# Kernel optimization log

Hardware: AMD Instinct MI355X
Metric: run time of the kernel (lower is better)

Reference implementation:

```python
import jax, jax.numpy as jnp
import numpy as np

N = 100000   # nodes
E = 1600000  # edges (avg degree 16)
D = 64       # feature / hidden / embedding dim
OUT = 2
NEG_SLOPE = 0.2


def setup_inputs() -> dict:
    key = jax.random.key(0)
    ks = jax.random.split(key, 12)
    s = 1.0 / np.sqrt(D)
    return {
        "x": jax.random.normal(ks[0], (N, D), dtype=jnp.float32),
        "edge_index": jax.random.randint(ks[1], (2, E), 0, N, dtype=jnp.int64),
        "Wl": jax.random.normal(ks[2], (3, D, D), dtype=jnp.float32) * s,
        "bl": jnp.zeros((3, D), dtype=jnp.float32),
        "Wr": jax.random.normal(ks[3], (3, D, D), dtype=jnp.float32) * s,
        "br": jnp.zeros((3, D), dtype=jnp.float32),
        "att": jax.random.normal(ks[4], (3, D), dtype=jnp.float32) * s,
        "bg": jnp.zeros((3, D), dtype=jnp.float32),
        "Ws": jax.random.normal(ks[5], (3, D, D), dtype=jnp.float32) * s,
        "bs": jnp.zeros((3, D), dtype=jnp.float32),
        "Wout": jax.random.normal(ks[6], (D, OUT), dtype=jnp.float32) * s,
        "bout": jnp.zeros((OUT,), dtype=jnp.float32),
    }


def _gatv2(h, src, dst, Wl, bl, Wr, br, att, bg):
    # GATv2Conv (heads=1, concat, add_self_loops=False):
    #   e_ij = att . LeakyReLU(Wl h_j + Wr h_i); softmax over incoming edges of i;
    #   out_i = sum_j alpha_ij * (Wl h_j) + bias
    xl = h @ Wl + bl                      # [N, D] source transform
    xr = h @ Wr + br                      # [N, D] dest transform
    e = jax.nn.leaky_relu(xl[src] + xr[dst], NEG_SLOPE) @ att  # [E]
    m = jax.ops.segment_max(e, dst, num_segments=N)            # per-dest max
    a = jnp.exp(e - m[dst])                                    # [E]
    denom = jax.ops.segment_sum(a, dst, num_segments=N)        # [N]
    alpha = a / denom[dst]                                     # [E]
    agg = jax.ops.segment_sum(alpha[:, None] * xl[src], dst, num_segments=N)
    return agg + bg                                            # [N, D]


def reference(x, edge_index, Wl, bl, Wr, br, att, bg, Ws, bs, Wout, bout):
    src, dst = edge_index[0], edge_index[1]
    # layer 1: gat1 + skip1, relu (dropout_rate=0 -> identity)
    h = jax.nn.relu(_gatv2(x, src, dst, Wl[0], bl[0], Wr[0], br[0], att[0], bg[0])
                    + x @ Ws[0] + bs[0])
    # middle layer
    h = jax.nn.relu(_gatv2(h, src, dst, Wl[1], bl[1], Wr[1], br[1], att[1], bg[1])
                    + h @ Ws[1] + bs[1])
    # last gat layer: no relu after
    h = _gatv2(h, src, dst, Wl[2], bl[2], Wr[2], br[2], att[2], bg[2]) + h @ Ws[2] + bs[2]
    return h @ Wout + bout
```

## Files before the change

kernel.cpp:

```cpp
#include <hip/hip_runtime.h>
#include <stdint.h>

#define NN 100000
#define EE 1600000
#define DD 64
#define NBUCK 391
#define SCWG 200
#define SCCHUNK 8000

using short8 = __attribute__((ext_vector_type(8))) short;
using f32x4  = __attribute__((ext_vector_type(4))) float;
using f2     = __attribute__((ext_vector_type(2))) float;


__device__ __forceinline__ unsigned short bf16_rne(float f) {
    unsigned int u = __float_as_uint(f);
    unsigned int r = (u + 0x7FFFu + ((u >> 16) & 1u)) >> 16;
    return (unsigned short)r;
}
__device__ __forceinline__ float bf16_to_f32(unsigned short h) {
    return __uint_as_float(((unsigned int)h) << 16);
}


__global__ void bucket_hist(const int* __restrict__ dst, int* __restrict__ bhist) {
    __shared__ int h[NBUCK];
    int t = threadIdx.x;
    for (int b = t; b < NBUCK; b += 256) h[b] = 0;
    __syncthreads();
    int start = blockIdx.x * SCCHUNK;
    int endi = min(start + SCCHUNK, EE);
    for (int e = start + t; e < endi; e += 256)
        atomicAdd(&h[dst[e] >> 8], 1);
    __syncthreads();
    for (int b = t; b < NBUCK; b += 256)
        if (h[b]) atomicAdd(&bhist[b], h[b]);
}

__global__ void bucket_scan(const int* __restrict__ bhist, int* __restrict__ bbase,
                            int* __restrict__ bcursor, int* __restrict__ offsets) {
    __shared__ int s[512];
    int t = threadIdx.x;
    int v = (t < NBUCK) ? bhist[t] : 0;
    s[t] = v;
    __syncthreads();
    for (int off = 1; off < 512; off <<= 1) {
        int a = (t >= off) ? s[t - off] : 0;
        __syncthreads();
        s[t] += a;
        __syncthreads();
    }
    if (t < NBUCK) { int excl = s[t] - v; bbase[t] = excl; bcursor[t] = excl; }
    if (t == 0) { bbase[NBUCK] = EE; offsets[NN] = EE; }
}

__global__ void bucket_scatter(const int* __restrict__ src, const int* __restrict__ dst,
                               int* __restrict__ bcursor, unsigned int* __restrict__ bedges) {
    __shared__ int cnt[NBUCK];
    __shared__ int lcur[NBUCK];
    int t = threadIdx.x;
    for (int b = t; b < NBUCK; b += 256) cnt[b] = 0;
    __syncthreads();
    int start = blockIdx.x * SCCHUNK;
    int endi = min(start + SCCHUNK, EE);
    for (int e = start + t; e < endi; e += 256)
        atomicAdd(&cnt[dst[e] >> 8], 1);
    __syncthreads();
    for (int b = t; b < NBUCK; b += 256) {
        int c = cnt[b];
        lcur[b] = c ? atomicAdd(&bcursor[b], c) : 0;
    }
    __syncthreads();
    for (int e = start + t; e < endi; e += 256) {
        int d = dst[e];
        int pos = atomicAdd(&lcur[d >> 8], 1);
        bedges[pos] = ((unsigned int)(d & 255) << 24) | (unsigned int)src[e];
    }
}

__global__ void bucket_csr(const unsigned int* __restrict__ bedges, const int* __restrict__ bbase,
                           int* __restrict__ offsets, int* __restrict__ csr) {
    __shared__ int ncnt[256];
    __shared__ int lofs[256];
    int b = blockIdx.x;
    int t = threadIdx.x;
    int beg = bbase[b], endb = bbase[b + 1];
    ncnt[t] = 0;
    __syncthreads();
    for (int e = beg + t; e < endb; e += 256)
        atomicAdd(&ncnt[bedges[e] >> 24], 1);
    __syncthreads();
    int v = ncnt[t];
    lofs[t] = v;
    __syncthreads();
    for (int off = 1; off < 256; off <<= 1) {
        int a = (t >= off) ? lofs[t - off] : 0;
        __syncthreads();
        lofs[t] += a;
        __syncthreads();
    }
    int excl = lofs[t] - v;
    int node = b * 256 + t;
    if (node < NN) offsets[node] = beg + excl;
    __syncthreads();
    ncnt[t] = beg + excl;
    __syncthreads();
    for (int e = beg + t; e < endb; e += 256) {
        unsigned int ed = bedges[e];
        int pos = atomicAdd(&ncnt[ed >> 24], 1);
        csr[pos] = (int)(ed & 0xFFFFFFu);
    }
}


__global__ void conv_wx(const float* __restrict__ Wl, const float* __restrict__ Wr,
                        const float* __restrict__ Ws, const float* __restrict__ x,
                        unsigned short* __restrict__ Wt_hi, unsigned short* __restrict__ Wt_lo,
                        unsigned short* __restrict__ Ahi) {
    if (blockIdx.x < 144) {
        int e = blockIdx.x * 256 + threadIdx.x;
        if (e >= 9 * 4096) return;
        int mat = e >> 12;
        int r   = e & 4095;
        int k   = r >> 6, n = r & 63;
        int L = mat / 3, j = mat % 3;
        const float* W = (j == 0) ? Wl : ((j == 1) ? Wr : Ws);
        float v = W[L * 4096 + k * 64 + n];
        unsigned short hi = bf16_rne(v);
        unsigned short lo = bf16_rne(v - bf16_to_f32(hi));
        Wt_hi[mat * 4096 + n * 64 + k] = hi;
        Wt_lo[mat * 4096 + n * 64 + k] = lo;
    } else {
        int i = (blockIdx.x - 144) * 256 + threadIdx.x;
        int total = NN * 16;
        int stride = (gridDim.x - 144) * 256;
        for (; i < total; i += stride) {
            float4 v = *(const float4*)&x[(size_t)i * 4];
            ushort4 h;
            h.x = bf16_rne(v.x);
            h.y = bf16_rne(v.y);
            h.z = bf16_rne(v.z);
            h.w = bf16_rne(v.w);
            *(ushort4*)&Ahi[(size_t)i * 4] = h;
        }
    }
}


__global__ __launch_bounds__(256) void gemm_mfma(
    const unsigned short* __restrict__ Ahi,
    const unsigned short* __restrict__ Wt_hi, const unsigned short* __restrict__ Wt_lo,
    const float* __restrict__ bl, const float* __restrict__ br, const float* __restrict__ bs,
    unsigned short* __restrict__ Xlb, unsigned short* __restrict__ XRS) {
    int lane = threadIdx.x & 63;
    int wid  = threadIdx.x >> 6;
    int m0 = (blockIdx.x * 4 + wid) * 32;
    if (m0 >= NN) return;

    int l4 = lane & 15;
    int hi = lane >> 4;
    int koff = hi * 8;

    int arow0 = m0 + l4, arow1 = m0 + 16 + l4;
    bool ok0 = arow0 < NN, ok1 = arow1 < NN;
    int ar0 = ok0 ? arow0 : NN - 1;
    int ar1 = ok1 ? arow1 : NN - 1;

    const unsigned short* ab0 = Ahi + (size_t)ar0 * 64;
    const unsigned short* ab1 = Ahi + (size_t)ar1 * 64;
    short8 a0k0 = *(const short8*)(ab0 + koff);
    short8 a0k1 = *(const short8*)(ab0 + 32 + koff);
    short8 a1k0 = *(const short8*)(ab1 + koff);
    short8 a1k1 = *(const short8*)(ab1 + 32 + koff);

    int nbase0 = hi * 4;

#pragma unroll
    for (int m = 0; m < 3; m++) {
        const unsigned short* wh = Wt_hi + m * 4096;
        const unsigned short* wl = Wt_lo + m * 4096;
        const float* bias = (m == 0) ? bl : ((m == 1) ? br : bs);
#pragma unroll
        for (int tt = 0; tt < 4; tt++) {
            int ncol = tt * 16 + l4;
            const unsigned short* bh = wh + ncol * 64 + koff;
            const unsigned short* blo = wl + ncol * 64 + koff;
            short8 bhi0 = *(const short8*)bh;
            short8 bhi1 = *(const short8*)(bh + 32);
            short8 blo0 = *(const short8*)blo;
            short8 blo1 = *(const short8*)(blo + 32);

            f32x4 acc0 = {0.f, 0.f, 0.f, 0.f};
            f32x4 acc1 = {0.f, 0.f, 0.f, 0.f};
            acc0 = __builtin_amdgcn_mfma_f32_16x16x32_bf16(bhi0, a0k0, acc0, 0, 0, 0);
            acc1 = __builtin_amdgcn_mfma_f32_16x16x32_bf16(bhi0, a1k0, acc1, 0, 0, 0);
            acc0 = __builtin_amdgcn_mfma_f32_16x16x32_bf16(bhi1, a0k1, acc0, 0, 0, 0);
            acc1 = __builtin_amdgcn_mfma_f32_16x16x32_bf16(bhi1, a1k1, acc1, 0, 0, 0);
            acc0 = __builtin_amdgcn_mfma_f32_16x16x32_bf16(blo0, a0k0, acc0, 0, 0, 0);
            acc1 = __builtin_amdgcn_mfma_f32_16x16x32_bf16(blo0, a1k0, acc1, 0, 0, 0);
            acc0 = __builtin_amdgcn_mfma_f32_16x16x32_bf16(blo1, a0k1, acc0, 0, 0, 0);
            acc1 = __builtin_amdgcn_mfma_f32_16x16x32_bf16(blo1, a1k1, acc1, 0, 0, 0);

            int nb = tt * 16 + nbase0;
            float4 bb = *(const float4*)&bias[nb];
            ushort4 h0, h1;
            h0.x = bf16_rne(acc0[0] + bb.x); h0.y = bf16_rne(acc0[1] + bb.y);
            h0.z = bf16_rne(acc0[2] + bb.z); h0.w = bf16_rne(acc0[3] + bb.w);
            h1.x = bf16_rne(acc1[0] + bb.x); h1.y = bf16_rne(acc1[1] + bb.y);
            h1.z = bf16_rne(acc1[2] + bb.z); h1.w = bf16_rne(acc1[3] + bb.w);
            if (m == 0) {
                if (ok0) *(ushort4*)&Xlb[(size_t)ar0 * 64 + nb] = h0;
                if (ok1) *(ushort4*)&Xlb[(size_t)ar1 * 64 + nb] = h1;
            } else {
                int coff = (m == 1) ? 0 : 64;
                if (ok0) *(ushort4*)&XRS[(size_t)ar0 * 128 + coff + nb] = h0;
                if (ok1) *(ushort4*)&XRS[(size_t)ar1 * 128 + coff + nb] = h1;
            }
        }
    }
}


__device__ __forceinline__ float group_sum16(float t) {
    t += __int_as_float(__builtin_amdgcn_update_dpp(0, __float_as_int(t), 0xB1, 0xF, 0xF, true));
    t += __int_as_float(__builtin_amdgcn_update_dpp(0, __float_as_int(t), 0x4E, 0xF, 0xF, true));
    t += __int_as_float(__builtin_amdgcn_update_dpp(0, __float_as_int(t), 0x141, 0xF, 0xF, true));
    t += __int_as_float(__builtin_amdgcn_update_dpp(0, __float_as_int(t), 0x140, 0xF, 0xF, true));
    return t;
}

__device__ __forceinline__ void unpack4(uint2 u, f2& v01, f2& v23) {
    v01 = f2{ __uint_as_float(u.x << 16), __uint_as_float(u.x & 0xFFFF0000u) };
    v23 = f2{ __uint_as_float(u.y << 16), __uint_as_float(u.y & 0xFFFF0000u) };
}

__global__ __launch_bounds__(256) void node_kernel(
    const unsigned short* __restrict__ Xlb, const unsigned short* __restrict__ XRS,
    const int* __restrict__ offsets, const int* __restrict__ csr,
    const float* __restrict__ att, const float* __restrict__ bg,
    unsigned short* __restrict__ hout, int do_relu,
    const float* __restrict__ Wout, const float* __restrict__ bout,
    float* __restrict__ outp, int do_out) {
    int lane = threadIdx.x & 63;
    int wid  = threadIdx.x >> 6;
    int i = blockIdx.x * 4 + wid;
    if (i >= NN) return;
    int sub = lane & 15;
    int grp = lane >> 4;

    f2 xr01, xr23;
    unpack4(*(const uint2*)&XRS[(size_t)i * 128 + sub * 4], xr01, xr23);
    float4 att4 = *(const float4*)&att[sub * 4];
    f2 at01 = {att4.x, att4.y}, at23 = {att4.z, att4.w};

    f2 agg01 = {0.f, 0.f}, agg23 = {0.f, 0.f};
    float denom = 0.f;
    int beg = offsets[i], end = offsets[i + 1];

    for (int j0 = beg; j0 < end; j0 += 8) {
        int jA = j0 + grp, jB = jA + 4;
        bool vA = jA < end, vB = jB < end;
        int sA = csr[vA ? jA : beg];
        int sB = csr[vB ? jB : beg];
        uint2 uA = *(const uint2*)&Xlb[(size_t)sA * 64 + sub * 4];
        uint2 uB = *(const uint2*)&Xlb[(size_t)sB * 64 + sub * 4];
        f2 xA01, xA23, xB01, xB23;
        unpack4(uA, xA01, xA23);
        unpack4(uB, xB01, xB23);

        f2 sA01 = xA01 + xr01;
        f2 sA23 = xA23 + xr23;
        f2 sB01 = xB01 + xr01;
        f2 sB23 = xB23 + xr23;
        f2 lA01 = { fmaxf(sA01.x, 0.2f * sA01.x), fmaxf(sA01.y, 0.2f * sA01.y) };
        f2 lA23 = { fmaxf(sA23.x, 0.2f * sA23.x), fmaxf(sA23.y, 0.2f * sA23.y) };
        f2 lB01 = { fmaxf(sB01.x, 0.2f * sB01.x), fmaxf(sB01.y, 0.2f * sB01.y) };
        f2 lB23 = { fmaxf(sB23.x, 0.2f * sB23.x), fmaxf(sB23.y, 0.2f * sB23.y) };

        f2 tAv = lA01 * at01 + lA23 * at23;
        f2 tBv = lB01 * at01 + lB23 * at23;
        float tA = group_sum16(tAv.x + tAv.y);
        float tB = group_sum16(tBv.x + tBv.y);
        float aA = vA ? __expf(tA) : 0.f;
        float aB = vB ? __expf(tB) : 0.f;

        f2 aAv = {aA, aA};
        f2 aBv = {aB, aB};
        agg01 += aAv * xA01 + aBv * xB01;
        agg23 += aAv * xA23 + aBv * xB23;
        denom += aA + aB;
    }

    float aggx = agg01.x, aggy = agg01.y, aggz = agg23.x, aggw = agg23.y;
#pragma unroll
    for (int m = 16; m <= 32; m <<= 1) {
        aggx  += __shfl_xor(aggx, m, 64);
        aggy  += __shfl_xor(aggy, m, 64);
        aggz  += __shfl_xor(aggz, m, 64);
        aggw  += __shfl_xor(aggw, m, 64);
        denom += __shfl_xor(denom, m, 64);
    }

    float inv = (denom > 0.f) ? (1.0f / denom) : 0.f;
    f2 sk01, sk23;
    unpack4(*(const uint2*)&XRS[(size_t)i * 128 + 64 + sub * 4], sk01, sk23);
    float4 bg4 = *(const float4*)&bg[sub * 4];
    float4 res;
    res.x = aggx * inv + bg4.x + sk01.x;
    res.y = aggy * inv + bg4.y + sk01.y;
    res.z = aggz * inv + bg4.z + sk23.x;
    res.w = aggw * inv + bg4.w + sk23.y;
    if (do_relu) {
        res.x = fmaxf(res.x, 0.f); res.y = fmaxf(res.y, 0.f);
        res.z = fmaxf(res.z, 0.f); res.w = fmaxf(res.w, 0.f);
    }
    if (do_out) {
        float4 w01 = *(const float4*)&Wout[8 * sub];
        float4 w23 = *(const float4*)&Wout[8 * sub + 4];
        float o0 = res.x * w01.x + res.y * w01.z + res.z * w23.x + res.w * w23.z;
        float o1 = res.x * w01.y + res.y * w01.w + res.z * w23.y + res.w * w23.w;
        o0 = group_sum16(o0);
        o1 = group_sum16(o1);
        if (lane == 0) {
            outp[(size_t)i * 2 + 0] = o0 + bout[0];
            outp[(size_t)i * 2 + 1] = o1 + bout[1];
        }
    } else {
        if (grp == 0) {
            ushort4 h;
            h.x = bf16_rne(res.x);
            h.y = bf16_rne(res.y);
            h.z = bf16_rne(res.z);
            h.w = bf16_rne(res.w);
            *(ushort4*)&hout[(size_t)i * 64 + sub * 4] = h;
        }
    }
}


extern "C" void kernel_launch(void* const* d_in, const int* in_sizes, int n_in,
                              void* d_out, int out_size, void* d_ws, size_t ws_size,
                              hipStream_t stream) {
    const float* x    = (const float*)d_in[0];
    const int*   ei   = (const int*)d_in[1];
    const float* Wl   = (const float*)d_in[2];
    const float* bl   = (const float*)d_in[3];
    const float* Wr   = (const float*)d_in[4];
    const float* br   = (const float*)d_in[5];
    const float* att  = (const float*)d_in[6];
    const float* bg   = (const float*)d_in[7];
    const float* Ws   = (const float*)d_in[8];
    const float* bs   = (const float*)d_in[9];
    const float* Wout = (const float*)d_in[10];
    const float* bout = (const float*)d_in[11];
    float* out = (float*)d_out;

    size_t off = 0;
    char* base = (char*)d_ws;
    auto alloc = [&](size_t bytes) -> void* {
        void* p = base + off;
        off += (bytes + 255) & ~(size_t)255;
        return p;
    };
    unsigned short* Xlb = (unsigned short*)alloc((size_t)NN * 64 * 2);
    unsigned short* XRS = (unsigned short*)alloc((size_t)NN * 128 * 2);
    unsigned short* Ahi = (unsigned short*)alloc((size_t)NN * 64 * 2);
    unsigned short* Bhi = (unsigned short*)alloc((size_t)NN * 64 * 2);
    unsigned short* Wthi = (unsigned short*)alloc((size_t)9 * 4096 * 2);
    unsigned short* Wtlo = (unsigned short*)alloc((size_t)9 * 4096 * 2);
    int*  bhist  = (int*)alloc((size_t)NBUCK * 4);
    int*  bbase  = (int*)alloc((size_t)(NBUCK + 1) * 4);
    int*  bcur   = (int*)alloc((size_t)NBUCK * 4);
    unsigned int* bedges = (unsigned int*)alloc((size_t)EE * 4);
    int*  offs   = (int*)alloc((size_t)(NN + 1) * 4);
    int*  csr    = (int*)alloc((size_t)EE * 4);

    const int* src = ei;
    const int* dst = ei + EE;

    hipMemsetAsync(bhist, 0, (size_t)NBUCK * 4, stream);
    bucket_hist<<<SCWG, 256, 0, stream>>>(dst, bhist);
    bucket_scan<<<1, 512, 0, stream>>>(bhist, bbase, bcur, offs);
    bucket_scatter<<<SCWG, 256, 0, stream>>>(src, dst, bcur, bedges);
    bucket_csr<<<NBUCK, 256, 0, stream>>>(bedges, bbase, offs, csr);

    conv_wx<<<144 + 400, 256, 0, stream>>>(Wl, Wr, Ws, x, Wthi, Wtlo, Ahi);

    unsigned short* cur = Ahi;
    unsigned short* nxt = Bhi;
    for (int L = 0; L < 3; L++) {
        gemm_mfma<<<(NN + 127) / 128, 256, 0, stream>>>(
            cur, Wthi + (size_t)L * 3 * 4096, Wtlo + (size_t)L * 3 * 4096,
            bl + L * 64, br + L * 64, bs + L * 64, Xlb, XRS);
        node_kernel<<<NN / 4, 256, 0, stream>>>(
            Xlb, XRS, offs, csr, att + L * 64, bg + L * 64,
            nxt, (L < 2) ? 1 : 0,
            Wout, bout, out, (L == 2) ? 1 : 0);
        unsigned short* tp = cur; cur = nxt; nxt = tp;
    }
}
```

Before: 340.4 us.

## Fuse histogram with conversion kernel, reuse per-block counts, widen node lanes

The dst-bucket histogram is merged into the weight/feature conversion kernel, and each block now writes its own partial histogram instead of updating a global array with atomics. The scan kernel sums the partials, and the scatter kernel reads its block's counts directly, so it no longer counts dst a second time. This also removes a memset and a launch. In the node kernel each edge is handled by 8 lanes with 8 features each (16-byte loads), giving 8 edges in flight per iteration instead of two groups of 4. The wider split uses shorter DPP reductions but needs more cross-group swizzle/shuffle reductions, and the serial 200-way sum in the scan adds latency.

```diff
diff --git a/kernel.cpp b/kernel.cpp
--- a/kernel.cpp
+++ b/kernel.cpp
@@ -21,104 +21,34 @@
 __device__ __forceinline__ float bf16_to_f32(unsigned short h) {
     return __uint_as_float(((unsigned int)h) << 16);
 }
-
-
-__global__ void bucket_hist(const int* __restrict__ dst, int* __restrict__ bhist) {
-    __shared__ int h[NBUCK];
-    int t = threadIdx.x;
-    for (int b = t; b < NBUCK; b += 256) h[b] = 0;
-    __syncthreads();
-    int start = blockIdx.x * SCCHUNK;
-    int endi = min(start + SCCHUNK, EE);
-    for (int e = start + t; e < endi; e += 256)
-        atomicAdd(&h[dst[e] >> 8], 1);
-    __syncthreads();
-    for (int b = t; b < NBUCK; b += 256)
-        if (h[b]) atomicAdd(&bhist[b], h[b]);
-}
-
-__global__ void bucket_scan(const int* __restrict__ bhist, int* __restrict__ bbase,
-                            int* __restrict__ bcursor, int* __restrict__ offsets) {
-    __shared__ int s[512];
-    int t = threadIdx.x;
-    int v = (t < NBUCK) ? bhist[t] : 0;
-    s[t] = v;
-    __syncthreads();
-    for (int off = 1; off < 512; off <<= 1) {
-        int a = (t >= off) ? s[t - off] : 0;
-        __syncthreads();
-        s[t] += a;
-        __syncthreads();
-    }
-    if (t < NBUCK) { int excl = s[t] - v; bbase[t] = excl; bcursor[t] = excl; }
-    if (t == 0) { bbase[NBUCK] = EE; offsets[NN] = EE; }
-}
-
-__global__ void bucket_scatter(const int* __restrict__ src, const int* __restrict__ dst,
-                               int* __restrict__ bcursor, unsigned int* __restrict__ bedges) {
-    __shared__ int cnt[NBUCK];
-    __shared__ int lcur[NBUCK];
-    int t = threadIdx.x;
-    for (int b = t; b < NBUCK; b += 256) cnt[b] = 0;
-    __syncthreads();
-    int start = blockIdx.x * SCCHUNK;
-    int endi = min(start + SCCHUNK, EE);
-    for (int e = start + t; e < endi; e += 256)
-        atomicAdd(&cnt[dst[e] >> 8], 1);
-    __syncthreads();
-    for (int b = t; b < NBUCK; b += 256) {
-        int c = cnt[b];
-        lcur[b] = c ? atomicAdd(&bcursor[b], c) : 0;
-    }
-    __syncthreads();
-    for (int e = start + t; e < endi; e += 256) {
-        int d = dst[e];
-        int pos = atomicAdd(&lcur[d >> 8], 1);
-        bedges[pos] = ((unsigned int)(d & 255) << 24) | (unsigned int)src[e];
-    }
-}
-
-__global__ void bucket_csr(const unsigned int* __restrict__ bedges, const int* __restrict__ bbase,
-                           int* __restrict__ offsets, int* __restrict__ csr) {
-    __shared__ int ncnt[256];
-    __shared__ int lofs[256];
+__device__ __forceinline__ void unpack8(uint4 u, f2& v0, f2& v1, f2& v2, f2& v3) {
+    v0 = f2{ __uint_as_float(u.x << 16), __uint_as_float(u.x & 0xFFFF0000u) };
+    v1 = f2{ __uint_as_float(u.y << 16), __uint_as_float(u.y & 0xFFFF0000u) };
+    v2 = f2{ __uint_as_float(u.z << 16), __uint_as_float(u.z & 0xFFFF0000u) };
+    v3 = f2{ __uint_as_float(u.w << 16), __uint_as_float(u.w & 0xFFFF0000u) };
+}
+
+
+__global__ void hist_conv(const int* __restrict__ dst, int* __restrict__ bhistPart,
+                          const float* __restrict__ Wl, const float* __restrict__ Wr,
+                          const float* __restrict__ Ws, const float* __restrict__ x,
+                          unsigned short* __restrict__ Wt_hi, unsigned short* __restrict__ Wt_lo,
+                          unsigned short* __restrict__ Ahi) {
     int b = blockIdx.x;
     int t = threadIdx.x;
-    int beg = bbase[b], endb = bbase[b + 1];
-    ncnt[t] = 0;
-    __syncthreads();
-    for (int e = beg + t; e < endb; e += 256)
-        atomicAdd(&ncnt[bedges[e] >> 24], 1);
-    __syncthreads();
-    int v = ncnt[t];
-    lofs[t] = v;
-    __syncthreads();
-    for (int off = 1; off < 256; off <<= 1) {
-        int a = (t >= off) ? lofs[t - off] : 0;
-        __syncthreads();
-        lofs[t] += a;
-        __syncthreads();
-    }
-    int excl = lofs[t] - v;
-    int node = b * 256 + t;
-    if (node < NN) offsets[node] = beg + excl;
-    __syncthreads();
-    ncnt[t] = beg + excl;
-    __syncthreads();
-    for (int e = beg + t; e < endb; e += 256) {
-        unsigned int ed = bedges[e];
-        int pos = atomicAdd(&ncnt[ed >> 24], 1);
-        csr[pos] = (int)(ed & 0xFFFFFFu);
-    }
-}
-
-
-__global__ void conv_wx(const float* __restrict__ Wl, const float* __restrict__ Wr,
-                        const float* __restrict__ Ws, const float* __restrict__ x,
-                        unsigned short* __restrict__ Wt_hi, unsigned short* __restrict__ Wt_lo,
-                        unsigned short* __restrict__ Ahi) {
-    if (blockIdx.x < 144) {
-        int e = blockIdx.x * 256 + threadIdx.x;
+    if (b < SCWG) {
+        __shared__ int h[NBUCK];
+        for (int i = t; i < NBUCK; i += 256) h[i] = 0;
+        __syncthreads();
+        int start = b * SCCHUNK;
+        int endi = min(start + SCCHUNK, EE);
+        for (int e = start + t; e < endi; e += 256)
+            atomicAdd(&h[dst[e] >> 8], 1);
+        __syncthreads();
+        for (int i = t; i < NBUCK; i += 256)
+            bhistPart[b * NBUCK + i] = h[i];
+    } else if (b < SCWG + 144) {
+        int e = (b - SCWG) * 256 + t;
         if (e >= 9 * 4096) return;
         int mat = e >> 12;
         int r   = e & 4095;
@@ -131,9 +61,9 @@
         Wt_hi[mat * 4096 + n * 64 + k] = hi;
         Wt_lo[mat * 4096 + n * 64 + k] = lo;
     } else {
-        int i = (blockIdx.x - 144) * 256 + threadIdx.x;
+        int i = (b - SCWG - 144) * 256 + t;
         int total = NN * 16;
-        int stride = (gridDim.x - 144) * 256;
+        int stride = (gridDim.x - SCWG - 144) * 256;
         for (; i < total; i += stride) {
             float4 v = *(const float4*)&x[(size_t)i * 4];
             ushort4 h;
@@ -143,6 +73,80 @@
             h.w = bf16_rne(v.w);
             *(ushort4*)&Ahi[(size_t)i * 4] = h;
         }
+    }
+}
+
+__global__ void bucket_scan(const int* __restrict__ bhistPart, int* __restrict__ bbase,
+                            int* __restrict__ bcursor, int* __restrict__ offsets) {
+    __shared__ int s[512];
+    int t = threadIdx.x;
+    int v = 0;
+    if (t < NBUCK) {
+        for (int w = 0; w < SCWG; w++) v += bhistPart[w * NBUCK + t];
+    }
+    s[t] = v;
+    __syncthreads();
+    for (int off = 1; off < 512; off <<= 1) {
+        int a = (t >= off) ? s[t - off] : 0;
+        __syncthreads();
+        s[t] += a;
+        __syncthreads();
+    }
+    if (t < NBUCK) { int excl = s[t] - v; bbase[t] = excl; bcursor[t] = excl; }
+    if (t == 0) { bbase[NBUCK] = EE; offsets[NN] = EE; }
+}
+
+__global__ void bucket_scatter(const int* __restrict__ src, const int* __restrict__ dst,
+                               const int* __restrict__ bhistPart,
+                               int* __restrict__ bcursor, unsigned int* __restrict__ bedges) {
+    __shared__ int lcur[NBUCK];
+    int t = threadIdx.x;
+    int b = blockIdx.x;
+    for (int i = t; i < NBUCK; i += 256) {
+        int c = bhistPart[b * NBUCK + i];
+        lcur[i] = c ? atomicAdd(&bcursor[i], c) : 0;
+    }
+    __syncthreads();
+    int start = b * SCCHUNK;
+    int endi = min(start + SCCHUNK, EE);
+    for (int e = start + t; e < endi; e += 256) {
+        int d = dst[e];
+        int pos = atomicAdd(&lcur[d >> 8], 1);
+        bedges[pos] = ((unsigned int)(d & 255) << 24) | (unsigned int)src[e];
+    }
+}
+
+__global__ void bucket_csr(const unsigned int* __restrict__ bedges, const int* __restrict__ bbase,
+                           int* __restrict__ offsets, int* __restrict__ csr) {
+    __shared__ int ncnt[256];
+    __shared__ int lofs[256];
+    int b = blockIdx.x;
+    int t = threadIdx.x;
+    int beg = bbase[b], endb = bbase[b + 1];
+    ncnt[t] = 0;
+    __syncthreads();
+    for (int e = beg + t; e < endb; e += 256)
+        atomicAdd(&ncnt[bedges[e] >> 24], 1);
+    __syncthreads();
+    int v = ncnt[t];
+    lofs[t] = v;
+    __syncthreads();
+    for (int off = 1; off < 256; off <<= 1) {
+        int a = (t >= off) ? lofs[t - off] : 0;
+        __syncthreads();
+        lofs[t] += a;
+        __syncthreads();
+    }
+    int excl = lofs[t] - v;
+    int node = b * 256 + t;
+    if (node < NN) offsets[node] = beg + excl;
+    __syncthreads();
+    ncnt[t] = beg + excl;
+    __syncthreads();
+    for (int e = beg + t; e < endb; e += 256) {
+        unsigned int ed = bedges[e];
+        int pos = atomicAdd(&ncnt[ed >> 24], 1);
+        csr[pos] = (int)(ed & 0xFFFFFFu);
     }
 }
 
@@ -221,17 +225,17 @@
 }
 
 
-__device__ __forceinline__ float group_sum16(float t) {
+__device__ __forceinline__ float group_sum8(float t) {
     t += __int_as_float(__builtin_amdgcn_update_dpp(0, __float_as_int(t), 0xB1, 0xF, 0xF, true));
     t += __int_as_float(__builtin_amdgcn_update_dpp(0, __float_as_int(t), 0x4E, 0xF, 0xF, true));
     t += __int_as_float(__builtin_amdgcn_update_dpp(0, __float_as_int(t), 0x141, 0xF, 0xF, true));
-    t += __int_as_float(__builtin_amdgcn_update_dpp(0, __float_as_int(t), 0x140, 0xF, 0xF, true));
     return t;
 }
-
-__device__ __forceinline__ void unpack4(uint2 u, f2& v01, f2& v23) {
-    v01 = f2{ __uint_as_float(u.x << 16), __uint_as_float(u.x & 0xFFFF0000u) };
-    v23 = f2{ __uint_as_float(u.y << 16), __uint_as_float(u.y & 0xFFFF0000u) };
+__device__ __forceinline__ float cross_group(float t) {
+    t += __int_as_float(__builtin_amdgcn_ds_swizzle(__float_as_int(t), 0x201F));
+    t += __int_as_float(__builtin_amdgcn_ds_swizzle(__float_as_int(t), 0x401F));
+    t += __shfl_xor(t, 32, 64);
+    return t;
 }
 
 __global__ __launch_bounds__(256) void node_kernel(
@@ -245,94 +249,93 @@
     int wid  = threadIdx.x >> 6;
     int i = blockIdx.x * 4 + wid;
     if (i >= NN) return;
-    int sub = lane & 15;
-    int grp = lane >> 4;
-
-    f2 xr01, xr23;
-    unpack4(*(const uint2*)&XRS[(size_t)i * 128 + sub * 4], xr01, xr23);
-    float4 att4 = *(const float4*)&att[sub * 4];
-    f2 at01 = {att4.x, att4.y}, at23 = {att4.z, att4.w};
-
-    f2 agg01 = {0.f, 0.f}, agg23 = {0.f, 0.f};
+    int sub = lane & 7;
+    int grp = lane >> 3;
+
+    f2 xr0, xr1, xr2, xr3;
+    unpack8(*(const uint4*)&XRS[(size_t)i * 128 + sub * 8], xr0, xr1, xr2, xr3);
+    float4 atA = *(const float4*)&att[sub * 8];
+    float4 atB = *(const float4*)&att[sub * 8 + 4];
+    f2 at0 = {atA.x, atA.y}, at1 = {atA.z, atA.w};
+    f2 at2 = {atB.x, atB.y}, at3 = {atB.z, atB.w};
+
+    f2 ag0 = {0.f, 0.f}, ag1 = {0.f, 0.f}, ag2 = {0.f, 0.f}, ag3 = {0.f, 0.f};
     float denom = 0.f;
     int beg = offsets[i], end = offsets[i + 1];
 
     for (int j0 = beg; j0 < end; j0 += 8) {
-        int jA = j0 + grp, jB = jA + 4;
-        bool vA = jA < end, vB = jB < end;
-        int sA = csr[vA ? jA : beg];
-        int sB = csr[vB ? jB : beg];
-        uint2 uA = *(const uint2*)&Xlb[(size_t)sA * 64 + sub * 4];
-        uint2 uB = *(const uint2*)&Xlb[(size_t)sB * 64 + sub * 4];
-        f2 xA01, xA23, xB01, xB23;
-        unpack4(uA, xA01, xA23);
-        unpack4(uB, xB01, xB23);
-
-        f2 sA01 = xA01 + xr01;
-        f2 sA23 = xA23 + xr23;
-        f2 sB01 = xB01 + xr01;
-        f2 sB23 = xB23 + xr23;
-        f2 lA01 = { fmaxf(sA01.x, 0.2f * sA01.x), fmaxf(sA01.y, 0.2f * sA01.y) };
-        f2 lA23 = { fmaxf(sA23.x, 0.2f * sA23.x), fmaxf(sA23.y, 0.2f * sA23.y) };
-        f2 lB01 = { fmaxf(sB01.x, 0.2f * sB01.x), fmaxf(sB01.y, 0.2f * sB01.y) };
-        f2 lB23 = { fmaxf(sB23.x, 0.2f * sB23.x), fmaxf(sB23.y, 0.2f * sB23.y) };
-
-        f2 tAv = lA01 * at01 + lA23 * at23;
-        f2 tBv = lB01 * at01 + lB23 * at23;
-        float tA = group_sum16(tAv.x + tAv.y);
-        float tB = group_sum16(tBv.x + tBv.y);
-        float aA = vA ? __expf(tA) : 0.f;
-        float aB = vB ? __expf(tB) : 0.f;
-
-        f2 aAv = {aA, aA};
-        f2 aBv = {aB, aB};
-        agg01 += aAv * xA01 + aBv * xB01;
-        agg23 += aAv * xA23 + aBv * xB23;
-        denom += aA + aB;
-    }
-
-    float aggx = agg01.x, aggy = agg01.y, aggz = agg23.x, aggw = agg23.y;
-#pragma unroll
-    for (int m = 16; m <= 32; m <<= 1) {
-        aggx  += __shfl_xor(aggx, m, 64);
-        aggy  += __shfl_xor(aggy, m, 64);
-        aggz  += __shfl_xor(aggz, m, 64);
-        aggw  += __shfl_xor(aggw, m, 64);
-        denom += __shfl_xor(denom, m, 64);
-    }
+        int jE = j0 + grp;
+        bool v = jE < end;
+        int sE = csr[v ? jE : beg];
+        f2 x0, x1, x2, x3;
+        unpack8(*(const uint4*)&Xlb[(size_t)sE * 64 + sub * 8], x0, x1, x2, x3);
+
+        f2 s0 = x0 + xr0, s1 = x1 + xr1, s2 = x2 + xr2, s3 = x3 + xr3;
+        f2 l0 = { fmaxf(s0.x, 0.2f * s0.x), fmaxf(s0.y, 0.2f * s0.y) };
+        f2 l1 = { fmaxf(s1.x, 0.2f * s1.x), fmaxf(s1.y, 0.2f * s1.y) };
+        f2 l2 = { fmaxf(s2.x, 0.2f * s2.x), fmaxf(s2.y, 0.2f * s2.y) };
+        f2 l3 = { fmaxf(s3.x, 0.2f * s3.x), fmaxf(s3.y, 0.2f * s3.y) };
+
+        f2 tv = l0 * at0 + l1 * at1;
+        tv += l2 * at2;
+        tv += l3 * at3;
+        float t = group_sum8(tv.x + tv.y);
+        float a = v ? __expf(t) : 0.f;
+
+        f2 av = {a, a};
+        ag0 += av * x0;
+        ag1 += av * x1;
+        ag2 += av * x2;
+        ag3 += av * x3;
+        denom += a;
+    }
+
+    float r0 = cross_group(ag0.x), r1 = cross_group(ag0.y);
+    float r2 = cross_group(ag1.x), r3 = cross_group(ag1.y);
+    float r4 = cross_group(ag2.x), r5 = cross_group(ag2.y);
+    float r6 = cross_group(ag3.x), r7 = cross_group(ag3.y);
+    denom = cross_group(denom);
 
     float inv = (denom > 0.f) ? (1.0f / denom) : 0.f;
-    f2 sk01, sk23;
-    unpack4(*(const uint2*)&XRS[(size_t)i * 128 + 64 + sub * 4], sk01, sk23);
-    float4 bg4 = *(const float4*)&bg[sub * 4];
-    float4 res;
-    res.x = aggx * inv + bg4.x + sk01.x;
-    res.y = aggy * inv + bg4.y + sk01.y;
-    res.z = aggz * inv + bg4.z + sk23.x;
-    res.w = aggw * inv + bg4.w + sk23.y;
+    f2 sk0, sk1, sk2, sk3;
+    unpack8(*(const uint4*)&XRS[(size_t)i * 128 + 64 + sub * 8], sk0, sk1, sk2, sk3);
+    float4 bgA = *(const float4*)&bg[sub * 8];
+    float4 bgB = *(const float4*)&bg[sub * 8 + 4];
+    float e0 = r0 * inv + bgA.x + sk0.x;
+    float e1 = r1 * inv + bgA.y + sk0.y;
+    float e2 = r2 * inv + bgA.z + sk1.x;
+    float e3 = r3 * inv + bgA.w + sk1.y;
+    float e4 = r4 * inv + bgB.x + sk2.x;
+    float e5 = r5 * inv + bgB.y + sk2.y;
+    float e6 = r6 * inv + bgB.z + sk3.x;
+    float e7 = r7 * inv + bgB.w + sk3.y;
     if (do_relu) {
-        res.x = fmaxf(res.x, 0.f); res.y = fmaxf(res.y, 0.f);
-        res.z = fmaxf(res.z, 0.f); res.w = fmaxf(res.w, 0.f);
+        e0 = fmaxf(e0, 0.f); e1 = fmaxf(e1, 0.f); e2 = fmaxf(e2, 0.f); e3 = fmaxf(e3, 0.f);
+        e4 = fmaxf(e4, 0.f); e5 = fmaxf(e5, 0.f); e6 = fmaxf(e6, 0.f); e7 = fmaxf(e7, 0.f);
     }
     if (do_out) {
-        float4 w01 = *(const float4*)&Wout[8 * sub];
-        float4 w23 = *(const float4*)&Wout[8 * sub + 4];
-        float o0 = res.x * w01.x + res.y * w01.z + res.z * w23.x + res.w * w23.z;
-        float o1 = res.x * w01.y + res.y * w01.w + res.z * w23.y + res.w * w23.w;
-        o0 = group_sum16(o0);
-        o1 = group_sum16(o1);
+        float4 wA = *(const float4*)&Wout[sub * 16];
+        float4 wB = *(const float4*)&Wout[sub * 16 + 4];
+        float4 wC = *(const float4*)&Wout[sub * 16 + 8];
+        float4 wD = *(const float4*)&Wout[sub * 16 + 12];
+        float o0 = e0 * wA.x + e1 * wA.z + e2 * wB.x + e3 * wB.z
+                 + e4 * wC.x + e5 * wC.z + e6 * wD.x + e7 * wD.z;
+        float o1 = e0 * wA.y + e1 * wA.w + e2 * wB.y + e3 * wB.w
+                 + e4 * wC.y + e5 * wC.w + e6 * wD.y + e7 * wD.w;
+        o0 = group_sum8(o0);
+        o1 = group_sum8(o1);
         if (lane == 0) {
             outp[(size_t)i * 2 + 0] = o0 + bout[0];
             outp[(size_t)i * 2 + 1] = o1 + bout[1];
         }
     } else {
         if (grp == 0) {
-            ushort4 h;
-            h.x = bf16_rne(res.x);
-            h.y = bf16_rne(res.y);
-            h.z = bf16_rne(res.z);
-            h.w = bf16_rne(res.w);
-            *(ushort4*)&hout[(size_t)i * 64 + sub * 4] = h;
+            uint4 hh;
+            hh.x = (unsigned)bf16_rne(e0) | ((unsigned)bf16_rne(e1) << 16);
+            hh.y = (unsigned)bf16_rne(e2) | ((unsigned)bf16_rne(e3) << 16);
+            hh.z = (unsigned)bf16_rne(e4) | ((unsigned)bf16_rne(e5) << 16);
+            hh.w = (unsigned)bf16_rne(e6) | ((unsigned)bf16_rne(e7) << 16);
+            *(uint4*)&hout[(size_t)i * 64 + sub * 8] = hh;
         }
     }
 }
@@ -368,7 +371,7 @@
     unsigned short* Bhi = (unsigned short*)alloc((size_t)NN * 64 * 2);
     unsigned short* Wthi = (unsigned short*)alloc((size_t)9 * 4096 * 2);
     unsigned short* Wtlo = (unsigned short*)alloc((size_t)9 * 4096 * 2);
-    int*  bhist  = (int*)alloc((size_t)NBUCK * 4);
+    int*  bhistPart = (int*)alloc((size_t)SCWG * NBUCK * 4);
     int*  bbase  = (int*)alloc((size_t)(NBUCK + 1) * 4);
     int*  bcur   = (int*)alloc((size_t)NBUCK * 4);
     unsigned int* bedges = (unsigned int*)alloc((size_t)EE * 4);
@@ -378,13 +381,11 @@
     const int* src = ei;
     const int* dst = ei + EE;
 
-    hipMemsetAsync(bhist, 0, (size_t)NBUCK * 4, stream);
-    bucket_hist<<<SCWG, 256, 0, stream>>>(dst, bhist);
-    bucket_scan<<<1, 512, 0, stream>>>(bhist, bbase, bcur, offs);
-    bucket_scatter<<<SCWG, 256, 0, stream>>>(src, dst, bcur, bedges);
+    hist_conv<<<SCWG + 144 + 400, 256, 0, stream>>>(dst, bhistPart, Wl, Wr, Ws, x,
+                                                    Wthi, Wtlo, Ahi);
+    bucket_scan<<<1, 512, 0, stream>>>(bhistPart, bbase, bcur, offs);
+    bucket_scatter<<<SCWG, 256, 0, stream>>>(src, dst, bhistPart, bcur, bedges);
     bucket_csr<<<NBUCK, 256, 0, stream>>>(bedges, bbase, offs, csr);
-
-    conv_wx<<<144 + 400, 256, 0, stream>>>(Wl, Wr, Ws, x, Wthi, Wtlo, Ahi);
 
     unsigned short* cur = Ahi;
     unsigned short* nxt = Bhi;
```

Result: no change. 336.0 us (-1.3%).
